# Kernel tuning notes

Measured on AMD Instinct MI355X. Metric: run time of the kernel, lower is better.

The kernel has to match this reference:

```python
import jax, jax.numpy as jnp
import numpy as np
from jax.scipy.linalg import expm

LATENT, HID, OMEGA, TRANZ, K = 64, 40, 9, 3, 262144


def _linear_params(key, out_d, in_d):
    # equinox Linear default init: U(-1/sqrt(in), 1/sqrt(in)) for weight and bias
    lim = 1.0 / np.sqrt(in_d)
    kw, kb = jax.random.split(key)
    W = jax.random.uniform(kw, (out_d, in_d), minval=-lim, maxval=lim, dtype=jnp.float32)
    b = jax.random.uniform(kb, (out_d,), minval=-lim, maxval=lim, dtype=jnp.float32)
    return W, b


def setup_inputs() -> dict:
    key = jax.random.key(0)
    keys = jax.random.split(key, 7)
    W_o1, b_o1 = _linear_params(keys[0], HID, LATENT)
    W_o2, b_o2 = _linear_params(keys[1], HID, HID)
    W_o3, b_o3 = _linear_params(keys[2], OMEGA, HID)
    W_t1, b_t1 = _linear_params(keys[3], HID, LATENT)
    W_t2, b_t2 = _linear_params(keys[4], HID, HID)
    W_t3, b_t3 = _linear_params(keys[5], TRANZ, HID)
    x = jax.random.normal(keys[6], (LATENT, K), dtype=jnp.float32)
    return {
        "x": x,
        "W_o1": W_o1, "b_o1": b_o1, "W_o2": W_o2, "b_o2": b_o2, "W_o3": W_o3, "b_o3": b_o3,
        "W_t1": W_t1, "b_t1": b_t1, "W_t2": W_t2, "b_t2": b_t2, "W_t3": W_t3, "b_t3": b_t3,
    }


def _exp_omega(omega_flat):
    # omega_flat: (9, K); expm of each column reshaped to 3x3, flattened -> (K, 9)
    f = lambda col: expm(col.reshape(3, 3)).reshape(9)
    return jax.vmap(f, in_axes=1)(omega_flat)


def reference(x, W_o1, b_o1, W_o2, b_o2, W_o3, b_o3,
              W_t1, b_t1, W_t2, b_t2, W_t3, b_t3):
    relu = jax.nn.relu
    # omega branch (note: original applies relu after EVERY layer, incl. last)
    h = relu(W_o1 @ x + b_o1[:, None])
    h = relu(W_o2 @ h + b_o2[:, None])
    omega = relu(W_o3 @ h + b_o3[:, None])          # (9, K)
    rotation = _exp_omega(omega).T                   # (9, K)
    # translation branch
    t = relu(W_t1 @ x + b_t1[:, None])
    t = relu(W_t2 @ t + b_t2[:, None])
    translation = relu(W_t3 @ t + b_t3[:, None])     # (3, K)
    return (omega, rotation, translation)
```

## Files before the change

kernel.cpp:

```cpp
#include <hip/hip_runtime.h>
#include <hip/hip_bf16.h>

#define KC 262144

typedef __attribute__((ext_vector_type(8))) short bf16x8;
typedef __attribute__((ext_vector_type(4))) float f32x4;
typedef unsigned short u16;
typedef unsigned int u32;

__device__ __forceinline__ u16 f2bf(float f) {
    u32 u = __float_as_uint(f);
    return (u16)((u + 0x7fffu + ((u >> 16) & 1u)) >> 16);
}
__device__ __forceinline__ u32 pk2(float a, float b) {
    u16 lo = __bfloat16_as_ushort(__float2bfloat16(a));
    u16 hi = __bfloat16_as_ushort(__float2bfloat16(b));
    return (u32)lo | ((u32)hi << 16);
}
__device__ __forceinline__ float bf2f(u32 h) {
    return __uint_as_float(h << 16);
}

__global__ __launch_bounds__(256) void prep(
    const float* __restrict__ Wo1, const float* __restrict__ bo1,
    const float* __restrict__ Wo2, const float* __restrict__ bo2,
    const float* __restrict__ Wo3, const float* __restrict__ bo3,
    const float* __restrict__ Wt1, const float* __restrict__ bt1,
    const float* __restrict__ Wt2, const float* __restrict__ bt2,
    const float* __restrict__ Wt3, const float* __restrict__ bt3,
    u16* __restrict__ ws)
{
    u16* W1s = ws;
    u16* W2s = ws + 5120;
    u16* W3s = ws + 12800;
    float* b1s = (float*)(ws + 14336);
    const int t0 = blockIdx.x * 256 + threadIdx.x;
    const int NT = gridDim.x * 256;

    for (int i = t0; i < 5120; i += NT) {
        int r = i >> 6, k = i & 63;
        float v = (r < 40) ? Wo1[r * 64 + k] : Wt1[(r - 40) * 64 + k];
        W1s[i] = f2bf(v);
    }
    for (int i = t0; i < 7680; i += NT) {
        int r = i / 96, k = i - r * 96;
        float v = 0.f;
        if (r < 40) {
            if (k < 40) v = Wo2[r * 40 + k];
            else if (k == 80) v = bo2[r];
        } else {
            int rr = r - 40;
            if (k >= 40 && k < 80) v = Wt2[rr * 40 + (k - 40)];
            else if (k == 80) v = bt2[rr];
        }
        W2s[i] = f2bf(v);
    }
    for (int i = t0; i < 1536; i += NT) {
        int r = i / 96, k = i - r * 96;
        float v = 0.f;
        if (r < 9) {
            if (k < 40) v = Wo3[r * 40 + k];
            else if (k == 80) v = bo3[r];
        } else if (r < 12) {
            int rr = r - 9;
            if (k >= 40 && k < 80) v = Wt3[rr * 40 + (k - 40)];
            else if (k == 80) v = bt3[rr];
        }
        W3s[i] = f2bf(v);
    }
    for (int i = t0; i < 80; i += NT)
        b1s[i] = (i < 40) ? bo1[i] : bt1[i - 40];
}

__device__ __forceinline__ void transpose_h(
    const u32* Px, const u32* Py, int g, int c, bf16x8* hb)
{
    const int srcA = 16 * (2 * (g & 1)) + c;
    const int srcB = srcA + 16;
    const bool hiM = (g >= 2);
#pragma unroll
    for (int s = 0; s < 2; ++s) {
        union { u32 u[4]; bf16x8 v; } uu;
        u32 a0 = (u32)__shfl((int)Px[2 * s], srcA);
        u32 b0 = (u32)__shfl((int)Px[2 * s + 1], srcA);
        uu.u[0] = hiM ? b0 : a0;
        u32 a1 = (u32)__shfl((int)Py[2 * s], srcA);
        u32 b1 = (u32)__shfl((int)Py[2 * s + 1], srcA);
        uu.u[1] = hiM ? b1 : a1;
        u32 a2 = (u32)__shfl((int)Px[2 * s], srcB);
        u32 b2 = (u32)__shfl((int)Px[2 * s + 1], srcB);
        uu.u[2] = hiM ? b2 : a2;
        u32 a3 = (u32)__shfl((int)Py[2 * s], srcB);
        u32 b3 = (u32)__shfl((int)Py[2 * s + 1], srcB);
        uu.u[3] = hiM ? b3 : a3;
        hb[s] = uu.v;
    }
    {
        union { u32 u[4]; bf16x8 v; } uu;
        u32 v0 = (u32)__shfl((int)Px[4], srcA);
        u32 v1 = (u32)__shfl((int)Py[4], srcA);
        u32 v2 = (u32)__shfl((int)Px[4], srcB);
        u32 v3 = (u32)__shfl((int)Py[4], srcB);
        u32 k0 = (g == 2) ? 0x00003f80u : 0u;
        uu.u[0] = hiM ? k0 : v0;
        uu.u[1] = hiM ? 0u : v1;
        uu.u[2] = hiM ? 0u : v2;
        uu.u[3] = hiM ? 0u : v3;
        hb[2] = uu.v;
    }
}

__global__ __launch_bounds__(256, 2) void mlp_shfl(
    const float* __restrict__ x, const u16* __restrict__ ws,
    float* __restrict__ out)
{
    const u16* W1s = ws;
    const u16* W2s = ws + 5120;
    const u16* W3s = ws + 12800;
    const float* b1s = (const float*)(ws + 14336);

    const int tid = threadIdx.x;
    const int wid = tid >> 6;
    const int lane = tid & 63;
    const int g = lane >> 4;
    const int c = lane & 15;
    const int wgid = blockIdx.x * 4 + wid;
    const int cbase = wgid * 64;

    bf16x8 A1[5][2], A3[3];
    f32x4 b1v[5];
#pragma unroll
    for (int m = 0; m < 5; ++m) {
#pragma unroll
        for (int s = 0; s < 2; ++s)
            A1[m][s] = *(const bf16x8*)(W1s + (16 * m + c) * 64 + 32 * s + 8 * g);
        b1v[m] = *(const f32x4*)(b1s + 16 * m + 4 * g);
    }
    bf16x8 A2[5][3];
#pragma unroll
    for (int m = 0; m < 5; ++m)
#pragma unroll
        for (int s = 0; s < 3; ++s)
            if (!(s == 0 && m >= 3))
                A2[m][s] = *(const bf16x8*)(W2s + (16 * m + c) * 96 + 32 * s + 8 * g);
#pragma unroll
    for (int s = 0; s < 3; ++s)
        A3[s] = *(const bf16x8*)(W3s + c * 96 + 32 * s + 8 * g);

    u32 xoff[16];
#pragma unroll
    for (int jj = 0; jj < 16; ++jj) {
        int row = 8 * g + (jj & 7) + 32 * (jj >> 3);
        xoff[jj] = (u32)((row * KC + cbase + c) * 4);
    }
    const char* xb_ = (const char*)x;

    float xr[16];
#pragma unroll
    for (int jj = 0; jj < 16; ++jj)
        xr[jj] = *(const float*)(xb_ + xoff[jj]);

    u32 w0[4], w1[4];

#pragma unroll
    for (int t = 0; t < 4; ++t) {
        bf16x8 xv[2];
#pragma unroll
        for (int s = 0; s < 2; ++s) {
            union { u32 u[4]; bf16x8 v; } uu;
#pragma unroll
            for (int p = 0; p < 4; ++p)
                uu.u[p] = pk2(xr[8 * s + 2 * p], xr[8 * s + 2 * p + 1]);
            xv[s] = uu.v;
        }

        float xrn[16];
        if (t < 3) {
#pragma unroll
            for (int jj = 0; jj < 16; ++jj)
                xrn[jj] = *(const float*)(xb_ + (xoff[jj] + (t + 1) * 64));
        }

        f32x4 a1[5];
#pragma unroll
        for (int m = 0; m < 5; ++m) a1[m] = b1v[m];
#pragma unroll
        for (int s = 0; s < 2; ++s)
#pragma unroll
            for (int m = 0; m < 5; ++m)
                a1[m] = __builtin_amdgcn_mfma_f32_16x16x32_bf16(
                    A1[m][s], xv[s], a1[m], 0, 0, 0);

        u32 Px[5], Py[5];
#pragma unroll
        for (int m = 0; m < 5; ++m) {
            Px[m] = pk2(fmaxf(a1[m][0], 0.f), fmaxf(a1[m][1], 0.f));
            Py[m] = pk2(fmaxf(a1[m][2], 0.f), fmaxf(a1[m][3], 0.f));
        }
        bf16x8 hb[3];
        transpose_h(Px, Py, g, c, hb);

        f32x4 a2[5];
#pragma unroll
        for (int m = 0; m < 5; ++m) a2[m] = f32x4{0.f, 0.f, 0.f, 0.f};
#pragma unroll
        for (int s = 0; s < 3; ++s)
#pragma unroll
            for (int m = 0; m < 5; ++m)
                if (!(s == 0 && m >= 3))
                    a2[m] = __builtin_amdgcn_mfma_f32_16x16x32_bf16(
                        A2[m][s], hb[s], a2[m], 0, 0, 0);
#pragma unroll
        for (int m = 0; m < 5; ++m) {
            Px[m] = pk2(fmaxf(a2[m][0], 0.f), fmaxf(a2[m][1], 0.f));
            Py[m] = pk2(fmaxf(a2[m][2], 0.f), fmaxf(a2[m][3], 0.f));
        }
        transpose_h(Px, Py, g, c, hb);

        f32x4 a3 = f32x4{0.f, 0.f, 0.f, 0.f};
#pragma unroll
        for (int s = 0; s < 3; ++s)
            a3 = __builtin_amdgcn_mfma_f32_16x16x32_bf16(
                A3[s], hb[s], a3, 0, 0, 0);

        w0[t] = pk2(fmaxf(a3[0], 0.f), fmaxf(a3[1], 0.f));
        w1[t] = pk2(fmaxf(a3[2], 0.f), fmaxf(a3[3], 0.f));

        if (t < 3) {
#pragma unroll
            for (int jj = 0; jj < 16; ++jj)
                xr[jj] = xrn[jj];
        }
    }

    {
        const int T = lane >> 4;
        const int cp = lane & 15;
        const int s0 = cp, s1 = 16 + cp, s2 = 32 + cp;

        auto selT = [&](u32 v0, u32 v1, u32 v2, u32 v3) -> u32 {
            u32 lo = (T & 1) ? v1 : v0;
            u32 hi = (T & 1) ? v3 : v2;
            return (T & 2) ? hi : lo;
        };
        u32 q0 = selT((u32)__shfl((int)w0[0], s0), (u32)__shfl((int)w0[1], s0),
                      (u32)__shfl((int)w0[2], s0), (u32)__shfl((int)w0[3], s0));
        u32 q1 = selT((u32)__shfl((int)w1[0], s0), (u32)__shfl((int)w1[1], s0),
                      (u32)__shfl((int)w1[2], s0), (u32)__shfl((int)w1[3], s0));
        u32 q2 = selT((u32)__shfl((int)w0[0], s1), (u32)__shfl((int)w0[1], s1),
                      (u32)__shfl((int)w0[2], s1), (u32)__shfl((int)w0[3], s1));
        u32 q3 = selT((u32)__shfl((int)w1[0], s1), (u32)__shfl((int)w1[1], s1),
                      (u32)__shfl((int)w1[2], s1), (u32)__shfl((int)w1[3], s1));
        u32 q4 = selT((u32)__shfl((int)w0[0], s2), (u32)__shfl((int)w0[1], s2),
                      (u32)__shfl((int)w0[2], s2), (u32)__shfl((int)w0[3], s2));
        u32 q5 = selT((u32)__shfl((int)w1[0], s2), (u32)__shfl((int)w1[1], s2),
                      (u32)__shfl((int)w1[2], s2), (u32)__shfl((int)w1[3], s2));

        float om[9];
        om[0] = bf2f(q0 & 0xffffu); om[1] = bf2f(q0 >> 16);
        om[2] = bf2f(q1 & 0xffffu); om[3] = bf2f(q1 >> 16);
        om[4] = bf2f(q2 & 0xffffu); om[5] = bf2f(q2 >> 16);
        om[6] = bf2f(q3 & 0xffffu); om[7] = bf2f(q3 >> 16);
        om[8] = bf2f(q4 & 0xffffu);
        float tr0 = bf2f(q4 >> 16);
        float tr1 = bf2f(q5 & 0xffffu);
        float tr2 = bf2f(q5 >> 16);

        const size_t ob = (size_t)cbase + lane;
#pragma unroll
        for (int j = 0; j < 9; ++j)
            out[(size_t)j * KC + ob] = om[j];
        out[(size_t)18 * KC + ob] = tr0;
        out[(size_t)19 * KC + ob] = tr1;
        out[(size_t)20 * KC + ob] = tr2;

        float B[9];
#pragma unroll
        for (int i = 0; i < 9; ++i) B[i] = om[i] * (1.0f / 32.0f);
        float T9[9] = {1.f, 0.f, 0.f, 0.f, 1.f, 0.f, 0.f, 0.f, 1.f};
#pragma unroll
        for (int m = 9; m >= 1; --m) {
            float U[9];
#pragma unroll
            for (int rr = 0; rr < 3; ++rr)
#pragma unroll
                for (int cc = 0; cc < 3; ++cc)
                    U[rr * 3 + cc] = B[rr * 3 + 0] * T9[0 * 3 + cc]
                                   + B[rr * 3 + 1] * T9[1 * 3 + cc]
                                   + B[rr * 3 + 2] * T9[2 * 3 + cc];
            const float s = 1.0f / (float)m;
#pragma unroll
            for (int i = 0; i < 9; ++i)
                T9[i] = U[i] * s + ((i == 0 || i == 4 || i == 8) ? 1.0f : 0.0f);
        }
#pragma unroll
        for (int q = 0; q < 5; ++q) {
            float U[9];
#pragma unroll
            for (int rr = 0; rr < 3; ++rr)
#pragma unroll
                for (int cc = 0; cc < 3; ++cc)
                    U[rr * 3 + cc] = T9[rr * 3 + 0] * T9[0 * 3 + cc]
                                   + T9[rr * 3 + 1] * T9[1 * 3 + cc]
                                   + T9[rr * 3 + 2] * T9[2 * 3 + cc];
#pragma unroll
            for (int i = 0; i < 9; ++i) T9[i] = U[i];
        }
#pragma unroll
        for (int j = 0; j < 9; ++j)
            out[(size_t)(9 + j) * KC + ob] = T9[j];
    }
}

extern "C" void kernel_launch(void* const* d_in, const int* in_sizes, int n_in,
                              void* d_out, int out_size, void* d_ws, size_t ws_size,
                              hipStream_t stream) {
    const float* x   = (const float*)d_in[0];
    const float* Wo1 = (const float*)d_in[1];
    const float* bo1 = (const float*)d_in[2];
    const float* Wo2 = (const float*)d_in[3];
    const float* bo2 = (const float*)d_in[4];
    const float* Wo3 = (const float*)d_in[5];
    const float* bo3 = (const float*)d_in[6];
    const float* Wt1 = (const float*)d_in[7];
    const float* bt1 = (const float*)d_in[8];
    const float* Wt2 = (const float*)d_in[9];
    const float* bt2 = (const float*)d_in[10];
    const float* Wt3 = (const float*)d_in[11];
    const float* bt3 = (const float*)d_in[12];

    u16* ws = (u16*)d_ws;
    float* out = (float*)d_out;

    hipLaunchKernelGGL(prep, dim3(16), dim3(256), 0, stream,
                       Wo1, bo1, Wo2, bo2, Wo3, bo3,
                       Wt1, bt1, Wt2, bt2, Wt3, bt3, ws);
    hipLaunchKernelGGL(mlp_shfl, dim3(1024), dim3(256), 0, stream,
                       x, ws, out);
}
```

Before: 35.09 us.

## Load x tiles via global_load_lds into LDS with double-half prefetch

Replaces per-lane scalar 4-byte global loads of x with 16-byte global_load_lds transfers into a per-wave LDS staging buffer. Each wave first loads half of its 64-column block, packs two tiles from LDS, then issues the second half's loads while computing the first two tiles. The aim is wider, more coalesced memory requests and overlap of the second load with MFMA work. It adds 32KB of LDS per block, which may limit occupancy, and relies on explicit waitcnt and sched barriers for correctness.

```diff
diff --git a/kernel.cpp b/kernel.cpp
--- a/kernel.cpp
+++ b/kernel.cpp
@@ -110,7 +110,7 @@
     }
 }
 
-__global__ __launch_bounds__(256, 2) void mlp_shfl(
+__global__ __launch_bounds__(256, 2) void mlp_glds(
     const float* __restrict__ x, const u16* __restrict__ ws,
     float* __restrict__ out)
 {
@@ -119,6 +119,8 @@
     const u16* W3s = ws + 12800;
     const float* b1s = (const float*)(ws + 14336);
 
+    __shared__ float stage[4][2048];
+
     const int tid = threadIdx.x;
     const int wid = tid >> 6;
     const int lane = tid & 63;
@@ -127,6 +129,18 @@
     const int wgid = blockIdx.x * 4 + wid;
     const int cbase = wgid * 64;
 
+    float* myst = &stage[wid][0];
+
+#pragma unroll
+    for (int i = 0; i < 8; ++i) {
+        const float* src = x + (size_t)(8 * i + (lane >> 3)) * KC
+                             + cbase + 4 * (lane & 7);
+        __builtin_amdgcn_global_load_lds(
+            (const __attribute__((address_space(1))) void*)src,
+            (__attribute__((address_space(3))) void*)(myst + i * 256),
+            16, 0, 0);
+    }
+
     bf16x8 A1[5][2], A3[3];
     f32x4 b1v[5];
 #pragma unroll
@@ -147,40 +161,22 @@
     for (int s = 0; s < 3; ++s)
         A3[s] = *(const bf16x8*)(W3s + c * 96 + 32 * s + 8 * g);
 
-    u32 xoff[16];
-#pragma unroll
-    for (int jj = 0; jj < 16; ++jj) {
-        int row = 8 * g + (jj & 7) + 32 * (jj >> 3);
-        xoff[jj] = (u32)((row * KC + cbase + c) * 4);
-    }
-    const char* xb_ = (const char*)x;
-
-    float xr[16];
-#pragma unroll
-    for (int jj = 0; jj < 16; ++jj)
-        xr[jj] = *(const float*)(xb_ + xoff[jj]);
-
-    u32 w0[4], w1[4];
-
-#pragma unroll
-    for (int t = 0; t < 4; ++t) {
-        bf16x8 xv[2];
+    const int loff = g * 256 + (c >> 2) * 4 + (c & 3);
+
+    auto pack_tile = [&](int tt, bf16x8 xv[2]) {
 #pragma unroll
         for (int s = 0; s < 2; ++s) {
             union { u32 u[4]; bf16x8 v; } uu;
 #pragma unroll
-            for (int p = 0; p < 4; ++p)
-                uu.u[p] = pk2(xr[8 * s + 2 * p], xr[8 * s + 2 * p + 1]);
+            for (int p = 0; p < 4; ++p) {
+                const float* a = myst + loff + s * 1024 + p * 64 + tt * 16;
+                uu.u[p] = pk2(a[0], a[32]);
+            }
             xv[s] = uu.v;
         }
-
-        float xrn[16];
-        if (t < 3) {
-#pragma unroll
-            for (int jj = 0; jj < 16; ++jj)
-                xrn[jj] = *(const float*)(xb_ + (xoff[jj] + (t + 1) * 64));
-        }
-
+    };
+
+    auto run_tile = [&](const bf16x8 xv[2], u32& o0, u32& o1) {
         f32x4 a1[5];
 #pragma unroll
         for (int m = 0; m < 5; ++m) a1[m] = b1v[m];
@@ -190,7 +186,6 @@
             for (int m = 0; m < 5; ++m)
                 a1[m] = __builtin_amdgcn_mfma_f32_16x16x32_bf16(
                     A1[m][s], xv[s], a1[m], 0, 0, 0);
-
         u32 Px[5], Py[5];
 #pragma unroll
         for (int m = 0; m < 5; ++m) {
@@ -222,16 +217,42 @@
         for (int s = 0; s < 3; ++s)
             a3 = __builtin_amdgcn_mfma_f32_16x16x32_bf16(
                 A3[s], hb[s], a3, 0, 0, 0);
-
-        w0[t] = pk2(fmaxf(a3[0], 0.f), fmaxf(a3[1], 0.f));
-        w1[t] = pk2(fmaxf(a3[2], 0.f), fmaxf(a3[3], 0.f));
-
-        if (t < 3) {
-#pragma unroll
-            for (int jj = 0; jj < 16; ++jj)
-                xr[jj] = xrn[jj];
-        }
-    }
+        o0 = pk2(fmaxf(a3[0], 0.f), fmaxf(a3[1], 0.f));
+        o1 = pk2(fmaxf(a3[2], 0.f), fmaxf(a3[3], 0.f));
+    };
+
+    u32 w0[4], w1[4];
+
+    asm volatile("s_waitcnt vmcnt(0)" ::: "memory");
+    __builtin_amdgcn_sched_barrier(0);
+
+    bf16x8 xv0[2], xv1[2];
+    pack_tile(0, xv0);
+    pack_tile(1, xv1);
+
+    asm volatile("s_waitcnt lgkmcnt(0)" ::: "memory");
+    __builtin_amdgcn_sched_barrier(0);
+
+#pragma unroll
+    for (int i = 0; i < 8; ++i) {
+        const float* src = x + (size_t)(8 * i + (lane >> 3)) * KC
+                             + cbase + 32 + 4 * (lane & 7);
+        __builtin_amdgcn_global_load_lds(
+            (const __attribute__((address_space(1))) void*)src,
+            (__attribute__((address_space(3))) void*)(myst + i * 256),
+            16, 0, 0);
+    }
+
+    run_tile(xv0, w0[0], w1[0]);
+    run_tile(xv1, w0[1], w1[1]);
+
+    asm volatile("s_waitcnt vmcnt(0)" ::: "memory");
+    __builtin_amdgcn_sched_barrier(0);
+
+    pack_tile(0, xv0);
+    pack_tile(1, xv1);
+    run_tile(xv0, w0[2], w1[2]);
+    run_tile(xv1, w0[3], w1[3]);
 
     {
         const int T = lane >> 4;
@@ -335,6 +356,6 @@
     hipLaunchKernelGGL(prep, dim3(16), dim3(256), 0, stream,
                        Wo1, bo1, Wo2, bo2, Wo3, bo3,
                        Wt1, bt1, Wt2, bt2, Wt3, bt3, ws);
-    hipLaunchKernelGGL(mlp_shfl, dim3(1024), dim3(256), 0, stream,
+    hipLaunchKernelGGL(mlp_glds, dim3(1024), dim3(256), 0, stream,
                        x, ws, out);
 }
```

Result: slower. 39.60 us (+12.8%).
